# Kernel optimization log

Measured on AMD Instinct MI355X. Metric: run time of the kernel, lower is better.

## Reference

```python
import jax, jax.numpy as jnp
import numpy as np

N = 100000
K = 5
ALPHA = 0.1
IN_DIM, HID_DIM, OUT_DIM = 512, 256, 64


def setup_inputs() -> dict:
    key = jax.random.key(0)
    k1, k2, k3, k4, k5, k6 = jax.random.split(key, 6)
    E = 3200000
    x = jax.random.normal(k1, (N, IN_DIM), dtype=jnp.float32)
    edge_index = jax.random.randint(k2, (2, E), 0, N, dtype=jnp.int32)
    s1 = 1.0 / np.sqrt(IN_DIM)
    s2 = 1.0 / np.sqrt(HID_DIM)
    W1 = jax.random.uniform(k3, (IN_DIM, HID_DIM), jnp.float32, -s1, s1)
    b1 = jax.random.uniform(k4, (HID_DIM,), jnp.float32, -s1, s1)
    W2 = jax.random.uniform(k5, (HID_DIM, OUT_DIM), jnp.float32, -s2, s2)
    b2 = jax.random.uniform(k6, (OUT_DIM,), jnp.float32, -s2, s2)
    return {"x": x, "edge_index": edge_index, "W1": W1, "b1": b1, "W2": W2, "b2": b2}


def _gcn_norm(edge_index, num_nodes):
    # add self loops, symmetric normalization D^-1/2 (A+I) D^-1/2
    loop = jnp.arange(num_nodes, dtype=edge_index.dtype)
    row = jnp.concatenate([edge_index[0], loop])
    col = jnp.concatenate([edge_index[1], loop])
    w = jnp.ones(row.shape[0], dtype=jnp.float32)
    deg = jax.ops.segment_sum(w, col, num_segments=num_nodes)
    dinv = jnp.where(deg > 0, jax.lax.rsqrt(deg), 0.0)
    norm = dinv[row] * w * dinv[col]
    return row, col, norm


def reference(x, edge_index, W1, b1, W2, b2):
    # MLP (dropout = identity in eval mode)
    h = jax.nn.relu(x @ W1 + b1) @ W2 + b2  # [N, OUT_DIM]
    row, col, norm = _gcn_norm(edge_index, N)
    x0 = h
    for _ in range(K):
        msg = h[row] * norm[:, None]                    # gather + scale [E+N, OUT_DIM]
        h = jax.ops.segment_sum(msg, col, num_segments=N)  # scatter-add
        h = (1.0 - ALPHA) * h + ALPHA * x0
    return jax.nn.log_softmax(h, axis=1)
```

## Files before the change

### kernel.cpp

```cpp
#include <hip/hip_runtime.h>

#define IN_DIM  512
#define HID_DIM 256
#define OUT_DIM 64
#define KPROP   5
#define ALPHA   0.1f

#define BKT_SHIFT 9
#define PART_EPB  8192

typedef short short8v __attribute__((ext_vector_type(8)));
typedef float f32x4   __attribute__((ext_vector_type(4)));
typedef float f32x2   __attribute__((ext_vector_type(2)));

__device__ __forceinline__ unsigned short f2bf(float f) {
    unsigned u = __builtin_bit_cast(unsigned, f);
    unsigned r = (u + 0x7FFFu + ((u >> 16) & 1u)) >> 16;
    return (unsigned short)r;
}
__device__ __forceinline__ float bflo(unsigned v) { return __builtin_bit_cast(float, v << 16); }
__device__ __forceinline__ float bfhi(unsigned v) { return __builtin_bit_cast(float, v & 0xffff0000u); }

__global__ __launch_bounds__(256) void bucket_count_kernel(const int* __restrict__ ei, int E,
                                                           int* __restrict__ bucketCnt) {
    __shared__ int hist[256];
    int t = threadIdx.x;
    hist[t] = 0;
    __syncthreads();
    int e0 = blockIdx.x * PART_EPB;
#pragma unroll 4
    for (int i = 0; i < PART_EPB / 256; ++i) {
        int e = e0 + i * 256 + t;
        if (e < E) atomicAdd(&hist[ei[E + e] >> BKT_SHIFT], 1);
    }
    __syncthreads();
    if (hist[t] > 0) atomicAdd(&bucketCnt[t], hist[t]);
}

__global__ __launch_bounds__(256) void bucket_scan_kernel(const int* __restrict__ bucketCnt,
                                                          int* __restrict__ bucketBase,
                                                          int* __restrict__ bucketFill,
                                                          int* __restrict__ indptr,
                                                          int E, int N) {
    __shared__ int sm[256];
    int t = threadIdx.x;
    int v = bucketCnt[t];
    sm[t] = v;
    __syncthreads();
    for (int off = 1; off < 256; off <<= 1) {
        int add = 0;
        if (t >= off) add = sm[t - off];
        __syncthreads();
        if (t >= off) sm[t] += add;
        __syncthreads();
    }
    int base = sm[t] - v;
    bucketBase[t] = base;
    bucketFill[t] = base;
    if (t == 0) indptr[N] = E;
}

__global__ __launch_bounds__(256) void partition_kernel(const int* __restrict__ ei, int E,
                                                        int* __restrict__ bucketFill,
                                                        int* __restrict__ packed) {
    __shared__ int hist[256];
    __shared__ int base[256];
    int t = threadIdx.x;
    int e0 = blockIdx.x * PART_EPB;
    hist[t] = 0;
    __syncthreads();
#pragma unroll 4
    for (int i = 0; i < PART_EPB / 256; ++i) {
        int e = e0 + i * 256 + t;
        if (e < E) atomicAdd(&hist[ei[E + e] >> BKT_SHIFT], 1);
    }
    __syncthreads();
    int cnt = hist[t];
    if (cnt > 0) base[t] = atomicAdd(&bucketFill[t], cnt);
    __syncthreads();
#pragma unroll 4
    for (int i = 0; i < PART_EPB / 256; ++i) {
        int e = e0 + i * 256 + t;
        if (e < E) {
            int dst = ei[E + e];
            int src = ei[e];
            int b = dst >> BKT_SHIFT;
            int pos = atomicAdd(&base[b], 1);
            packed[pos] = ((dst & 511) << 17) | src;
        }
    }
}

__global__ __launch_bounds__(256) void fine_kernel(const int* __restrict__ packed,
                                                   const int* __restrict__ bucketBase,
                                                   const int* __restrict__ bucketCnt,
                                                   int* __restrict__ csr_row,
                                                   int* __restrict__ indptr,
                                                   float* __restrict__ dinv, int N) {
    __shared__ int cnt[512];
    __shared__ int pre[512];
    __shared__ int fill[512];
    __shared__ int sm[256];
    int b = blockIdx.x;
    int t = threadIdx.x;
    int d0 = b << BKT_SHIFT;
    int nd = N - d0;
    if (nd > 512) nd = 512;
    cnt[t] = 0; cnt[t + 256] = 0;
    fill[t] = 0; fill[t + 256] = 0;
    __syncthreads();
    int beg = bucketBase[b];
    int end = beg + bucketCnt[b];
    for (int e = beg + t; e < end; e += 256)
        atomicAdd(&cnt[((unsigned)packed[e]) >> 17], 1);
    __syncthreads();
    int c0 = cnt[2 * t], c1 = cnt[2 * t + 1];
    int s = c0 + c1;
    sm[t] = s;
    __syncthreads();
    for (int off = 1; off < 256; off <<= 1) {
        int add = 0;
        if (t >= off) add = sm[t - off];
        __syncthreads();
        if (t >= off) sm[t] += add;
        __syncthreads();
    }
    int ex = sm[t] - s;
    pre[2 * t] = ex;
    pre[2 * t + 1] = ex + c0;
    __syncthreads();
    for (int dl = t; dl < nd; dl += 256) {
        indptr[d0 + dl] = beg + pre[dl];
        dinv[d0 + dl] = rsqrtf((float)(cnt[dl] + 1));
    }
    for (int e = beg + t; e < end; e += 256) {
        unsigned p = (unsigned)packed[e];
        int dl = (int)(p >> 17);
        int src = (int)(p & 0x1FFFFu);
        int pos = beg + pre[dl] + atomicAdd(&fill[dl], 1);
        csr_row[pos] = src;
    }
}

__global__ __launch_bounds__(256) void prep_w1_kernel(const float* __restrict__ W1,
                                                      unsigned short* __restrict__ w1p) {
    int idx = blockIdx.x * 256 + threadIdx.x;
    int q = idx >> 14;
    int rem = idx & 16383;
    int c = rem >> 6, j = rem & 63;
    w1p[idx] = f2bf(W1[(size_t)(q * 64 + j) * HID_DIM + c]);
}

__global__ __launch_bounds__(256) void prep_w2_kernel(const float* __restrict__ W2,
                                                      unsigned short* __restrict__ w2p) {
    int idx = blockIdx.x * 256 + threadIdx.x;
    int c = idx >> 8, k = idx & 255;
    w2p[idx] = f2bf(W2[(size_t)k * OUT_DIM + c]);
}

struct __align__(16) MlpSmem {
    union {
        struct {
            unsigned short xs[64][72];
            unsigned short ws[256][72];
        } p1;
        struct {
            unsigned short hid[64][264];
            unsigned short w2s[32][264];
        } p2;
    };
};

__device__ __forceinline__ float4 ldx1(const float* __restrict__ x, int row0, int N,
                                       int t, int i, int q) {
    int e = t * 4 + i * 1024;
    int r = e >> 6, j = e & 63;
    if (row0 + r < N) return *(const float4*)&x[(size_t)(row0 + r) * IN_DIM + q * 64 + j];
    return make_float4(0.f, 0.f, 0.f, 0.f);
}

__global__ __launch_bounds__(256, 3) void mlp_mfma_kernel(const float* __restrict__ x,
                                                          const unsigned short* __restrict__ w1p,
                                                          const float* __restrict__ b1,
                                                          const unsigned short* __restrict__ w2p,
                                                          const float* __restrict__ b2,
                                                          const float* __restrict__ dinv,
                                                          unsigned short* __restrict__ zb,
                                                          unsigned char* __restrict__ hs,
                                                          int N) {
    __shared__ MlpSmem sm;
    int t = threadIdx.x;
    int w = t >> 6, l = t & 63;
    int l15 = l & 15, l4 = l >> 4;
    int wr0 = w * 16;
    int row0 = blockIdx.x * 64;

    f32x4 acc[16];
#pragma unroll
    for (int i = 0; i < 16; ++i) acc[i] = (f32x4){0.f, 0.f, 0.f, 0.f};

    float4 xr0, xr1, xr2, xr3;
    uint4 wv0, wv1, wv2, wv3, wv4, wv5, wv6, wv7;

#define LOADX(q) do { \
        xr0 = ldx1(x, row0, N, t, 0, (q)); \
        xr1 = ldx1(x, row0, N, t, 1, (q)); \
        xr2 = ldx1(x, row0, N, t, 2, (q)); \
        xr3 = ldx1(x, row0, N, t, 3, (q)); \
    } while (0)
#define LOADW(q) do { \
        const unsigned short* _s = w1p + (q) * 16384; \
        wv0 = *(const uint4*)&_s[t * 8 + 0 * 2048]; \
        wv1 = *(const uint4*)&_s[t * 8 + 1 * 2048]; \
        wv2 = *(const uint4*)&_s[t * 8 + 2 * 2048]; \
        wv3 = *(const uint4*)&_s[t * 8 + 3 * 2048]; \
        wv4 = *(const uint4*)&_s[t * 8 + 4 * 2048]; \
        wv5 = *(const uint4*)&_s[t * 8 + 5 * 2048]; \
        wv6 = *(const uint4*)&_s[t * 8 + 6 * 2048]; \
        wv7 = *(const uint4*)&_s[t * 8 + 7 * 2048]; \
    } while (0)
#define STX(i, v) do { \
        int e = t * 4 + (i) * 1024; \
        int r = e >> 6, j = e & 63; \
        unsigned u0 = (unsigned)f2bf((v).x) | ((unsigned)f2bf((v).y) << 16); \
        unsigned u1 = (unsigned)f2bf((v).z) | ((unsigned)f2bf((v).w) << 16); \
        *(uint2*)&sm.p1.xs[r][j] = make_uint2(u0, u1); \
    } while (0)
#define STW(i, v) do { \
        int e = t * 8 + (i) * 2048; \
        int c = e >> 6, j = e & 63; \
        *(uint4*)&sm.p1.ws[c][j] = (v); \
    } while (0)

    LOADX(0);
    LOADW(0);

    for (int q = 0; q < 8; ++q) {
        __syncthreads();
        STX(0, xr0); STX(1, xr1); STX(2, xr2); STX(3, xr3);
        STW(0, wv0); STW(1, wv1); STW(2, wv2); STW(3, wv3);
        STW(4, wv4); STW(5, wv5); STW(6, wv6); STW(7, wv7);
        __syncthreads();
        if (q < 7) {
            LOADX(q + 1);
            LOADW(q + 1);
        }
#pragma unroll
        for (int s = 0; s < 2; ++s) {
            short8v a = *(const short8v*)&sm.p1.xs[wr0 + l15][s * 32 + l4 * 8];
#pragma unroll
            for (int tc = 0; tc < 16; ++tc) {
                short8v b = *(const short8v*)&sm.p1.ws[tc * 16 + l15][s * 32 + l4 * 8];
                acc[tc] = __builtin_amdgcn_mfma_f32_16x16x32_bf16(a, b, acc[tc], 0, 0, 0);
            }
        }
    }
    __syncthreads();

#pragma unroll
    for (int tc = 0; tc < 16; ++tc) {
        float bv = b1[tc * 16 + l15];
#pragma unroll
        for (int i = 0; i < 4; ++i) {
            float v = fmaxf(acc[tc][i] + bv, 0.f);
            sm.p2.hid[wr0 + l4 * 4 + i][tc * 16 + l15] = f2bf(v);
        }
    }

    f32x4 acc2[4];
#pragma unroll
    for (int i = 0; i < 4; ++i) acc2[i] = (f32x4){0.f, 0.f, 0.f, 0.f};

#pragma unroll
    for (int hf = 0; hf < 2; ++hf) {
#pragma unroll
        for (int i = 0; i < 4; ++i) {
            int e = t * 8 + i * 2048;
            int c = e >> 8, k = e & 255;
            *(uint4*)&sm.p2.w2s[c][k] = *(const uint4*)&w2p[hf * 8192 + e];
        }
        __syncthreads();
#pragma unroll
        for (int s = 0; s < 8; ++s) {
            short8v a = *(const short8v*)&sm.p2.hid[wr0 + l15][s * 32 + l4 * 8];
#pragma unroll
            for (int tcl = 0; tcl < 2; ++tcl) {
                short8v b = *(const short8v*)&sm.p2.w2s[tcl * 16 + l15][s * 32 + l4 * 8];
                acc2[hf * 2 + tcl] =
                    __builtin_amdgcn_mfma_f32_16x16x32_bf16(a, b, acc2[hf * 2 + tcl], 0, 0, 0);
            }
        }
        __syncthreads();
    }

#pragma unroll
    for (int i = 0; i < 4; ++i) {
        int row = row0 + wr0 + l4 * 4 + i;
        if (row < N) {
            float dv = dinv[row];
#pragma unroll
            for (int tc = 0; tc < 4; ++tc) {
                float v = acc2[tc][i] + b2[tc * 16 + l15];
                zb[(size_t)row * OUT_DIM + tc * 16 + l15] = f2bf(ALPHA * v);
                float sv = dv * v;
                int pk = __builtin_amdgcn_cvt_pk_fp8_f32(sv, sv, 0, false);
                hs[(size_t)row * OUT_DIM + tc * 16 + l15] = (unsigned char)(pk & 0xFF);
            }
        }
    }
#undef LOADX
#undef LOADW
#undef STX
#undef STW
}

__global__ __launch_bounds__(256) void prop_fp8_kernel(const unsigned char* __restrict__ hs,
                                                       const unsigned short* __restrict__ zb,
                                                       const float* __restrict__ dinv,
                                                       const int* __restrict__ csr_row,
                                                       const int* __restrict__ indptr,
                                                       unsigned char* __restrict__ hs_out,
                                                       float* __restrict__ hfin,
                                                       int last, int N) {
    int node = blockIdx.x * 4 + (threadIdx.x >> 6);
    if (node >= N) return;
    int l = threadIdx.x & 63;
    int q8 = l >> 3, lf8 = l & 7;
    const uint2* H2 = (const uint2*)hs;
    int beg = indptr[node], end = indptr[node + 1];
    float b0 = 0.f, b1v = 0.f, b2v = 0.f, b3 = 0.f;
    float b4 = 0.f, b5 = 0.f, b6 = 0.f, b7 = 0.f;
#define ACCU2(u2) do { \
        f32x2 _p0 = __builtin_amdgcn_cvt_pk_f32_fp8((int)(u2).x, false); \
        f32x2 _p1 = __builtin_amdgcn_cvt_pk_f32_fp8((int)(u2).x, true);  \
        f32x2 _p2 = __builtin_amdgcn_cvt_pk_f32_fp8((int)(u2).y, false); \
        f32x2 _p3 = __builtin_amdgcn_cvt_pk_f32_fp8((int)(u2).y, true);  \
        b0 += _p0[0]; b1v += _p0[1]; b2v += _p1[0]; b3 += _p1[1];        \
        b4 += _p2[0]; b5 += _p2[1]; b6 += _p3[0]; b7 += _p3[1];          \
    } while (0)
    int e = beg;
    for (; e + 32 <= end; e += 32) {
        int r0 = csr_row[e + 0 + q8];
        int r1 = csr_row[e + 8 + q8];
        int r2 = csr_row[e + 16 + q8];
        int r3 = csr_row[e + 24 + q8];
        uint2 u0 = H2[(size_t)r0 * 8 + lf8];
        uint2 u1 = H2[(size_t)r1 * 8 + lf8];
        uint2 u2 = H2[(size_t)r2 * 8 + lf8];
        uint2 u3 = H2[(size_t)r3 * 8 + lf8];
        ACCU2(u0); ACCU2(u1); ACCU2(u2); ACCU2(u3);
    }
    for (; e + 8 <= end; e += 8) {
        int r = csr_row[e + q8];
        uint2 u = H2[(size_t)r * 8 + lf8];
        ACCU2(u);
    }
    if (e + q8 < end) {
        int r = csr_row[e + q8];
        uint2 u = H2[(size_t)r * 8 + lf8];
        ACCU2(u);
    }
    b0 += __shfl_xor(b0, 8);  b1v += __shfl_xor(b1v, 8);
    b2v += __shfl_xor(b2v, 8); b3 += __shfl_xor(b3, 8);
    b4 += __shfl_xor(b4, 8);  b5 += __shfl_xor(b5, 8);
    b6 += __shfl_xor(b6, 8);  b7 += __shfl_xor(b7, 8);
    b0 += __shfl_xor(b0, 16); b1v += __shfl_xor(b1v, 16);
    b2v += __shfl_xor(b2v, 16); b3 += __shfl_xor(b3, 16);
    b4 += __shfl_xor(b4, 16); b5 += __shfl_xor(b5, 16);
    b6 += __shfl_xor(b6, 16); b7 += __shfl_xor(b7, 16);
    b0 += __shfl_xor(b0, 32); b1v += __shfl_xor(b1v, 32);
    b2v += __shfl_xor(b2v, 32); b3 += __shfl_xor(b3, 32);
    b4 += __shfl_xor(b4, 32); b5 += __shfl_xor(b5, 32);
    b6 += __shfl_xor(b6, 32); b7 += __shfl_xor(b7, 32);
    {
        uint2 us = H2[(size_t)node * 8 + lf8];
        ACCU2(us);
    }
#undef ACCU2
    float dcn = dinv[node];
    uint4 zv = ((const uint4*)zb)[(size_t)node * 8 + lf8];
    float o0 = (1.0f - ALPHA) * (dcn * b0) + bflo(zv.x);
    float o1 = (1.0f - ALPHA) * (dcn * b1v) + bfhi(zv.x);
    float o2 = (1.0f - ALPHA) * (dcn * b2v) + bflo(zv.y);
    float o3 = (1.0f - ALPHA) * (dcn * b3) + bfhi(zv.y);
    float o4 = (1.0f - ALPHA) * (dcn * b4) + bflo(zv.z);
    float o5 = (1.0f - ALPHA) * (dcn * b5) + bfhi(zv.z);
    float o6 = (1.0f - ALPHA) * (dcn * b6) + bflo(zv.w);
    float o7 = (1.0f - ALPHA) * (dcn * b7) + bfhi(zv.w);
    if (last) {
        float m = fmaxf(fmaxf(fmaxf(o0, o1), fmaxf(o2, o3)),
                        fmaxf(fmaxf(o4, o5), fmaxf(o6, o7)));
        m = fmaxf(m, __shfl_xor(m, 1));
        m = fmaxf(m, __shfl_xor(m, 2));
        m = fmaxf(m, __shfl_xor(m, 4));
        float s = expf(o0 - m) + expf(o1 - m) + expf(o2 - m) + expf(o3 - m) +
                  expf(o4 - m) + expf(o5 - m) + expf(o6 - m) + expf(o7 - m);
        s += __shfl_xor(s, 1);
        s += __shfl_xor(s, 2);
        s += __shfl_xor(s, 4);
        float lg = logf(s);
        if (q8 == 0) {
            float4 oa, ob;
            oa.x = o0 - m - lg; oa.y = o1 - m - lg; oa.z = o2 - m - lg; oa.w = o3 - m - lg;
            ob.x = o4 - m - lg; ob.y = o5 - m - lg; ob.z = o6 - m - lg; ob.w = o7 - m - lg;
            *(float4*)&hfin[(size_t)node * 64 + lf8 * 8] = oa;
            *(float4*)&hfin[(size_t)node * 64 + lf8 * 8 + 4] = ob;
        }
    } else if (q8 == 0) {
        int pk0 = __builtin_amdgcn_cvt_pk_fp8_f32(dcn * o0, dcn * o1, 0, false);
        pk0 = __builtin_amdgcn_cvt_pk_fp8_f32(dcn * o2, dcn * o3, pk0, true);
        int pk1 = __builtin_amdgcn_cvt_pk_fp8_f32(dcn * o4, dcn * o5, 0, false);
        pk1 = __builtin_amdgcn_cvt_pk_fp8_f32(dcn * o6, dcn * o7, pk1, true);
        ((uint2*)hs_out)[(size_t)node * 8 + lf8] = make_uint2((unsigned)pk0, (unsigned)pk1);
    }
}

extern "C" void kernel_launch(void* const* d_in, const int* in_sizes, int n_in,
                              void* d_out, int out_size, void* d_ws, size_t ws_size,
                              hipStream_t stream) {
    const float* x  = (const float*)d_in[0];
    const int*   ei = (const int*)d_in[1];
    const float* W1 = (const float*)d_in[2];
    const float* b1 = (const float*)d_in[3];
    const float* W2 = (const float*)d_in[4];
    const float* b2 = (const float*)d_in[5];
    float* out = (float*)d_out;
    int N = in_sizes[0] / IN_DIM;
    int E = in_sizes[1] / 2;
    int nbkt = (N + 511) >> BKT_SHIFT;

    char* ws = (char*)d_ws;
    size_t off = 0;
    auto alloc = [&](size_t bytes) -> void* {
        void* p = ws + off;
        off += (bytes + 255) & ~(size_t)255;
        return p;
    };
    unsigned short* zb = (unsigned short*)alloc((size_t)N * OUT_DIM * 2);
    float* dinv   = (float*)alloc((size_t)N * 4);
    int*   indptr = (int*)alloc((size_t)(N + 1) * 4);
    int*   bcnt   = (int*)alloc(256 * 4);
    int*   bbase  = (int*)alloc(256 * 4);
    int*   bfill  = (int*)alloc(256 * 4);
    int*   packed = (int*)alloc((size_t)E * 4);
    int*   csr_row= (int*)alloc((size_t)E * 4);
    unsigned short* w1p = (unsigned short*)alloc((size_t)IN_DIM * HID_DIM * 2);
    unsigned short* w2p = (unsigned short*)alloc((size_t)HID_DIM * OUT_DIM * 2);
    unsigned char* hsA = (unsigned char*)alloc((size_t)N * OUT_DIM);
    unsigned char* hsB = (unsigned char*)alloc((size_t)N * OUT_DIM);
    (void)ws_size; (void)n_in; (void)out_size;

    hipMemsetAsync(bcnt, 0, 256 * 4, stream);

    prep_w1_kernel<<<(IN_DIM * HID_DIM) / 256, 256, 0, stream>>>(W1, w1p);
    prep_w2_kernel<<<(HID_DIM * OUT_DIM) / 256, 256, 0, stream>>>(W2, w2p);

    int pgrid = (E + PART_EPB - 1) / PART_EPB;
    bucket_count_kernel<<<pgrid, 256, 0, stream>>>(ei, E, bcnt);
    bucket_scan_kernel<<<1, 256, 0, stream>>>(bcnt, bbase, bfill, indptr, E, N);
    partition_kernel<<<pgrid, 256, 0, stream>>>(ei, E, bfill, packed);
    fine_kernel<<<nbkt, 256, 0, stream>>>(packed, bbase, bcnt, csr_row, indptr, dinv, N);

    mlp_mfma_kernel<<<(N + 63) / 64, 256, 0, stream>>>(x, w1p, b1, w2p, b2, dinv,
                                                       zb, hsA, N);

    int pb = (N + 3) / 4;
    for (int it = 0; it < KPROP; ++it) {
        const unsigned char* hin = (it % 2 == 0) ? hsA : hsB;
        unsigned char* hout = (it % 2 == 0) ? hsB : hsA;
        int last = (it == KPROP - 1) ? 1 : 0;
        prop_fp8_kernel<<<pb, 256, 0, stream>>>(hin, zb, dinv, csr_row, indptr,
                                                hout, out, last, N);
    }
}
```

Measured before the change: 457.2 us.

## Split MLP kernel across 8 waves with column-split accumulators and double-buffered x loads

The MLP kernel moves from 256 to 512 threads per block. Waves now split the 256 hidden columns in two, which halves per-thread accumulators and register pressure and should raise occupancy. The K loop is unrolled by two with alternating x register sets, so global loads for the next chunks are in flight while the current chunk runs its MFMAs. W2 is staged in one shot with a larger shared buffer. This adds shared-memory use and more barriers per block.

Measured after the change: 458.6 us. No clear change (+0.3%).

```diff
diff --git a/kernel.cpp b/kernel.cpp
--- a/kernel.cpp
+++ b/kernel.cpp
@@ -166,20 +166,20 @@
         } p1;
         struct {
             unsigned short hid[64][264];
-            unsigned short w2s[32][264];
+            unsigned short w2s[64][264];
         } p2;
     };
 };
 
-__device__ __forceinline__ float4 ldx1(const float* __restrict__ x, int row0, int N,
-                                       int t, int i, int q) {
-    int e = t * 4 + i * 1024;
+__device__ __forceinline__ float4 ldx512(const float* __restrict__ x, int row0, int N,
+                                         int t, int i, int q) {
+    int e = t * 4 + i * 2048;
     int r = e >> 6, j = e & 63;
     if (row0 + r < N) return *(const float4*)&x[(size_t)(row0 + r) * IN_DIM + q * 64 + j];
     return make_float4(0.f, 0.f, 0.f, 0.f);
 }
 
-__global__ __launch_bounds__(256, 3) void mlp_mfma_kernel(const float* __restrict__ x,
+__global__ __launch_bounds__(512, 4) void mlp_mfma_kernel(const float* __restrict__ x,
                                                           const unsigned short* __restrict__ w1p,
                                                           const float* __restrict__ b1,
                                                           const unsigned short* __restrict__ w2p,
@@ -192,105 +192,101 @@
     int t = threadIdx.x;
     int w = t >> 6, l = t & 63;
     int l15 = l & 15, l4 = l >> 4;
-    int wr0 = w * 16;
+    int wr0 = (w & 3) * 16;
+    int wc = w >> 2;
     int row0 = blockIdx.x * 64;
 
-    f32x4 acc[16];
-#pragma unroll
-    for (int i = 0; i < 16; ++i) acc[i] = (f32x4){0.f, 0.f, 0.f, 0.f};
-
-    float4 xr0, xr1, xr2, xr3;
-    uint4 wv0, wv1, wv2, wv3, wv4, wv5, wv6, wv7;
-
-#define LOADX(q) do { \
-        xr0 = ldx1(x, row0, N, t, 0, (q)); \
-        xr1 = ldx1(x, row0, N, t, 1, (q)); \
-        xr2 = ldx1(x, row0, N, t, 2, (q)); \
-        xr3 = ldx1(x, row0, N, t, 3, (q)); \
-    } while (0)
+    f32x4 acc[8];
+#pragma unroll
+    for (int i = 0; i < 8; ++i) acc[i] = (f32x4){0.f, 0.f, 0.f, 0.f};
+
+    float4 xa0, xa1, xb0, xb1;
+    uint4 wv0, wv1, wv2, wv3;
+
+#define LOADXA(q) do { xa0 = ldx512(x, row0, N, t, 0, (q)); xa1 = ldx512(x, row0, N, t, 1, (q)); } while (0)
+#define LOADXB(q) do { xb0 = ldx512(x, row0, N, t, 0, (q)); xb1 = ldx512(x, row0, N, t, 1, (q)); } while (0)
 #define LOADW(q) do { \
         const unsigned short* _s = w1p + (q) * 16384; \
-        wv0 = *(const uint4*)&_s[t * 8 + 0 * 2048]; \
-        wv1 = *(const uint4*)&_s[t * 8 + 1 * 2048]; \
-        wv2 = *(const uint4*)&_s[t * 8 + 2 * 2048]; \
-        wv3 = *(const uint4*)&_s[t * 8 + 3 * 2048]; \
-        wv4 = *(const uint4*)&_s[t * 8 + 4 * 2048]; \
-        wv5 = *(const uint4*)&_s[t * 8 + 5 * 2048]; \
-        wv6 = *(const uint4*)&_s[t * 8 + 6 * 2048]; \
-        wv7 = *(const uint4*)&_s[t * 8 + 7 * 2048]; \
+        wv0 = *(const uint4*)&_s[t * 8 + 0 * 4096]; \
+        wv1 = *(const uint4*)&_s[t * 8 + 1 * 4096]; \
+        wv2 = *(const uint4*)&_s[t * 8 + 2 * 4096]; \
+        wv3 = *(const uint4*)&_s[t * 8 + 3 * 4096]; \
     } while (0)
-#define STX(i, v) do { \
-        int e = t * 4 + (i) * 1024; \
+#define STX1(i, v) do { \
+        int e = t * 4 + (i) * 2048; \
         int r = e >> 6, j = e & 63; \
         unsigned u0 = (unsigned)f2bf((v).x) | ((unsigned)f2bf((v).y) << 16); \
         unsigned u1 = (unsigned)f2bf((v).z) | ((unsigned)f2bf((v).w) << 16); \
         *(uint2*)&sm.p1.xs[r][j] = make_uint2(u0, u1); \
     } while (0)
-#define STW(i, v) do { \
-        int e = t * 8 + (i) * 2048; \
+#define STW1(i, v) do { \
+        int e = t * 8 + (i) * 4096; \
         int c = e >> 6, j = e & 63; \
         *(uint4*)&sm.p1.ws[c][j] = (v); \
     } while (0)
-
-    LOADX(0);
+#define MFMA_CHUNK() do { \
+        _Pragma("unroll") \
+        for (int s = 0; s < 2; ++s) { \
+            short8v a = *(const short8v*)&sm.p1.xs[wr0 + l15][s * 32 + l4 * 8]; \
+            _Pragma("unroll") \
+            for (int tc = 0; tc < 8; ++tc) { \
+                short8v b = *(const short8v*)&sm.p1.ws[wc * 128 + tc * 16 + l15][s * 32 + l4 * 8]; \
+                acc[tc] = __builtin_amdgcn_mfma_f32_16x16x32_bf16(a, b, acc[tc], 0, 0, 0); \
+            } \
+        } \
+    } while (0)
+
+    LOADXA(0);
+    LOADXB(1);
     LOADW(0);
 
-    for (int q = 0; q < 8; ++q) {
-        __syncthreads();
-        STX(0, xr0); STX(1, xr1); STX(2, xr2); STX(3, xr3);
-        STW(0, wv0); STW(1, wv1); STW(2, wv2); STW(3, wv3);
-        STW(4, wv4); STW(5, wv5); STW(6, wv6); STW(7, wv7);
-        __syncthreads();
-        if (q < 7) {
-            LOADX(q + 1);
-            LOADW(q + 1);
-        }
-#pragma unroll
-        for (int s = 0; s < 2; ++s) {
-            short8v a = *(const short8v*)&sm.p1.xs[wr0 + l15][s * 32 + l4 * 8];
-#pragma unroll
-            for (int tc = 0; tc < 16; ++tc) {
-                short8v b = *(const short8v*)&sm.p1.ws[tc * 16 + l15][s * 32 + l4 * 8];
-                acc[tc] = __builtin_amdgcn_mfma_f32_16x16x32_bf16(a, b, acc[tc], 0, 0, 0);
-            }
-        }
-    }
-    __syncthreads();
-
-#pragma unroll
-    for (int tc = 0; tc < 16; ++tc) {
-        float bv = b1[tc * 16 + l15];
+#pragma unroll
+    for (int q = 0; q < 8; q += 2) {
+        __syncthreads();
+        STX1(0, xa0); STX1(1, xa1);
+        STW1(0, wv0); STW1(1, wv1); STW1(2, wv2); STW1(3, wv3);
+        __syncthreads();
+        if (q + 2 < 8) LOADXA(q + 2);
+        LOADW(q + 1);
+        MFMA_CHUNK();
+        __syncthreads();
+        STX1(0, xb0); STX1(1, xb1);
+        STW1(0, wv0); STW1(1, wv1); STW1(2, wv2); STW1(3, wv3);
+        __syncthreads();
+        if (q + 3 < 8) LOADXB(q + 3);
+        if (q + 2 < 8) LOADW(q + 2);
+        MFMA_CHUNK();
+    }
+    __syncthreads();
+
+#pragma unroll
+    for (int tc = 0; tc < 8; ++tc) {
+        float bv = b1[wc * 128 + tc * 16 + l15];
 #pragma unroll
         for (int i = 0; i < 4; ++i) {
             float v = fmaxf(acc[tc][i] + bv, 0.f);
-            sm.p2.hid[wr0 + l4 * 4 + i][tc * 16 + l15] = f2bf(v);
+            sm.p2.hid[wr0 + l4 * 4 + i][wc * 128 + tc * 16 + l15] = f2bf(v);
         }
     }
-
-    f32x4 acc2[4];
-#pragma unroll
-    for (int i = 0; i < 4; ++i) acc2[i] = (f32x4){0.f, 0.f, 0.f, 0.f};
-
-#pragma unroll
-    for (int hf = 0; hf < 2; ++hf) {
-#pragma unroll
-        for (int i = 0; i < 4; ++i) {
-            int e = t * 8 + i * 2048;
-            int c = e >> 8, k = e & 255;
-            *(uint4*)&sm.p2.w2s[c][k] = *(const uint4*)&w2p[hf * 8192 + e];
+#pragma unroll
+    for (int i = 0; i < 4; ++i) {
+        int e = t * 8 + i * 4096;
+        int c = e >> 8, k = e & 255;
+        *(uint4*)&sm.p2.w2s[c][k] = *(const uint4*)&w2p[e];
+    }
+    __syncthreads();
+
+    f32x4 acc2[2];
+#pragma unroll
+    for (int i = 0; i < 2; ++i) acc2[i] = (f32x4){0.f, 0.f, 0.f, 0.f};
+#pragma unroll
+    for (int s = 0; s < 8; ++s) {
+        short8v a = *(const short8v*)&sm.p2.hid[wr0 + l15][s * 32 + l4 * 8];
+#pragma unroll
+        for (int tcl = 0; tcl < 2; ++tcl) {
+            short8v b = *(const short8v*)&sm.p2.w2s[wc * 32 + tcl * 16 + l15][s * 32 + l4 * 8];
+            acc2[tcl] = __builtin_amdgcn_mfma_f32_16x16x32_bf16(a, b, acc2[tcl], 0, 0, 0);
         }
-        __syncthreads();
-#pragma unroll
-        for (int s = 0; s < 8; ++s) {
-            short8v a = *(const short8v*)&sm.p2.hid[wr0 + l15][s * 32 + l4 * 8];
-#pragma unroll
-            for (int tcl = 0; tcl < 2; ++tcl) {
-                short8v b = *(const short8v*)&sm.p2.w2s[tcl * 16 + l15][s * 32 + l4 * 8];
-                acc2[hf * 2 + tcl] =
-                    __builtin_amdgcn_mfma_f32_16x16x32_bf16(a, b, acc2[hf * 2 + tcl], 0, 0, 0);
-            }
-        }
-        __syncthreads();
     }
 
 #pragma unroll
@@ -299,19 +295,22 @@
         if (row < N) {
             float dv = dinv[row];
 #pragma unroll
-            for (int tc = 0; tc < 4; ++tc) {
-                float v = acc2[tc][i] + b2[tc * 16 + l15];
-                zb[(size_t)row * OUT_DIM + tc * 16 + l15] = f2bf(ALPHA * v);
+            for (int tcl = 0; tcl < 2; ++tcl) {
+                int col = wc * 32 + tcl * 16 + l15;
+                float v = acc2[tcl][i] + b2[col];
+                zb[(size_t)row * OUT_DIM + col] = f2bf(ALPHA * v);
                 float sv = dv * v;
                 int pk = __builtin_amdgcn_cvt_pk_fp8_f32(sv, sv, 0, false);
-                hs[(size_t)row * OUT_DIM + tc * 16 + l15] = (unsigned char)(pk & 0xFF);
+                hs[(size_t)row * OUT_DIM + col] = (unsigned char)(pk & 0xFF);
             }
         }
     }
-#undef LOADX
+#undef LOADXA
+#undef LOADXB
 #undef LOADW
-#undef STX
-#undef STW
+#undef STX1
+#undef STW1
+#undef MFMA_CHUNK
 }
 
 __global__ __launch_bounds__(256) void prop_fp8_kernel(const unsigned char* __restrict__ hs,
@@ -461,7 +460,7 @@
     partition_kernel<<<pgrid, 256, 0, stream>>>(ei, E, bfill, packed);
     fine_kernel<<<nbkt, 256, 0, stream>>>(packed, bbase, bcnt, csr_row, indptr, dinv, N);
 
-    mlp_mfma_kernel<<<(N + 63) / 64, 256, 0, stream>>>(x, w1p, b1, w2p, b2, dinv,
+    mlp_mfma_kernel<<<(N + 63) / 64, 512, 0, stream>>>(x, w1p, b1, w2p, b2, dinv,
                                                        zb, hsA, N);
 
     int pb = (N + 3) / 4;
```
